# Performance work log

Measured on AMD Instinct MI355X. Metric: run time of the kernel, lower is better.

Reference implementation:

```python
import jax, jax.numpy as jnp
import numpy as np

PATCH = 5
DIM = 256
HEADS = 8
EPS = 1e-5


def split_patches(t, p):
    # t: [B,H,W,C] -> overlapping patches [B,H,W,p,p,C], stride 1, zero-pad p//2
    pad = p // 2
    tp = jnp.pad(t, ((0, 0), (pad, pad), (pad, pad), (0, 0)))
    H, W = t.shape[1], t.shape[2]
    rows = jnp.arange(H)[:, None] + jnp.arange(p)[None, :]  # [H,p]
    cols = jnp.arange(W)[:, None] + jnp.arange(p)[None, :]  # [W,p]
    return tp[:, rows[:, None, :, None], cols[None, :, None, :], :]


def layernorm(v, g, b):
    mu = jnp.mean(v, axis=-1, keepdims=True)
    var = jnp.var(v, axis=-1, keepdims=True)
    return (v - mu) * jax.lax.rsqrt(var + EPS) * g + b


def mha(q, k, v, w, b, mask):
    # w: [4,D,D] stacked (Wq,Wk,Wv,Wo), b: [4,D]; q:[N,Lq,D], k,v:[N,Lk,D]
    N, Lq, D = q.shape
    dh = D // HEADS
    qh = (q @ w[0] + b[0]).reshape(N, Lq, HEADS, dh)
    kh = (k @ w[1] + b[1]).reshape(N, -1, HEADS, dh)
    vh = (v @ w[2] + b[2]).reshape(N, -1, HEADS, dh)
    sc = jnp.einsum('nqhd,nkhd->nhqk', qh, kh) * (1.0 / float(np.sqrt(dh)))
    if mask is not None:
        sc = jnp.where(mask, sc, jnp.asarray(-1e9, sc.dtype))
    a = jax.nn.softmax(sc, axis=-1)
    o = jnp.einsum('nhqk,nkhd->nqhd', a, vh).reshape(N, Lq, D)
    return o @ w[3] + b[3], a


def setup_inputs() -> dict:
    key = jax.random.key(0)
    ks = jax.random.split(key, 10)
    B, H, W, D = 1, 64, 64, DIM
    x = jax.random.normal(ks[0], (B, H, W, D), dtype=jnp.float32)
    memory = jax.random.normal(ks[1], (B, H, W, D), dtype=jnp.float32)
    active_nodes = jax.random.randint(ks[2], (B, H, W), 0, 2).astype(bool)
    s = 0.05
    return {
        'x': x, 'memory': memory, 'active_nodes': active_nodes,
        'attn_w': jax.random.normal(ks[3], (4, D, D), dtype=jnp.float32) * s,
        'attn_b': jnp.zeros((4, D), dtype=jnp.float32),
        'pattn_w': jax.random.normal(ks[4], (4, D, D), dtype=jnp.float32) * s,
        'pattn_b': jnp.zeros((4, D), dtype=jnp.float32),
        'ff_w1': jax.random.normal(ks[5], (D, 2 * D), dtype=jnp.float32) * s,
        'ff_b1': jnp.zeros((2 * D,), dtype=jnp.float32),
        'ff_w2': jax.random.normal(ks[6], (2 * D, D), dtype=jnp.float32) * s,
        'ff_b2': jnp.zeros((D,), dtype=jnp.float32),
        'ln_g': jnp.ones((3, D), dtype=jnp.float32),   # norm1, norm2, norm3
        'ln_b': jnp.zeros((3, D), dtype=jnp.float32),
    }


def reference(x, memory, active_nodes, attn_w, attn_b, pattn_w, pattn_b,
              ff_w1, ff_b1, ff_w2, ff_b2, ln_g, ln_b):
    B, H, W, D = x.shape
    p = PATCH
    center = p // 2
    L = p * p
    cp = L // 2  # flattened center point

    act = active_nodes[..., None]                      # [B,H,W,1] bool
    ap = split_patches(act, p)                         # [B,H,W,p,p,1]
    # faithful to source: zeroes the entire patch at GRID position (center,center)
    ap = ap.at[:, center, center].set(False)
    wo_center = jnp.any(ap.reshape(B, H, W, L, 1), axis=3)  # [B,H,W,1]
    act = jnp.logical_and(wo_center, act)
    ap = split_patches(act, p)                         # recomputed with updated mask

    xp = split_patches(x, p) * ap                      # zero inactive neighbors
    xp = xp.reshape(B, H, W, L, D)
    mp = split_patches(memory, p).reshape(B, H, W, L, D)
    mask = ap[..., 0].reshape(B, H, W, L)

    N = B * H * W
    keys = xp.reshape(N, L, D)
    mem = mp.reshape(N, L, D)
    q = keys[:, cp:cp + 1, :]                          # [N,1,D]
    m = mask.reshape(N, L)[:, None, None, :]           # [N,1,1,L]

    # EncoderLayer (eval mode: dropout = identity)
    s_, attn = mha(q, keys, keys, attn_w, attn_b, m)
    s = layernorm(q + s_, ln_g[0], ln_b[0])            # norm1
    s_, _ = mha(s, mem, mem, pattn_w, pattn_b, None)
    s = layernorm(s + s_, ln_g[2], ln_b[2])            # norm3
    ff = jax.nn.relu(s @ ff_w1 + ff_b1) @ ff_w2 + ff_b2
    s = layernorm(s + ff, ln_g[1], ln_b[1])            # norm2

    out = jnp.where(act, s[:, 0, :].reshape(B, H, W, D), jnp.asarray(0.0, x.dtype))
    return out, act[..., 0]
```

## Files before the change

### kernel.cpp

```cpp
#include <hip/hip_runtime.h>
#include <math.h>

#define D 256
#define H2 512
#define HEADS 8
#define L 25
#define GH 64
#define GW 64
#define NN 4096
#define EPS 1e-5f
#define SCALE 0.17677669529663687f
#define NND 1048576

typedef __attribute__((ext_vector_type(8))) short short8;
typedef __attribute__((ext_vector_type(4))) short short4v;
typedef __attribute__((ext_vector_type(4))) float f32x4;

__device__ __forceinline__ bool act_at(const int* __restrict__ active, int h, int w) {
    if (h < 0 || h >= GH || w < 0 || w >= GW) return false;
    if (h == 2 && w == 2) return false;
    return active[h * GW + w] != 0;
}

__device__ __forceinline__ unsigned short f2b(float f) {
    unsigned u = __float_as_uint(f);
    u += 0x7fffu + ((u >> 16) & 1u);
    return (unsigned short)(u >> 16);
}
__device__ __forceinline__ float b2f(short v) {
    return __uint_as_float(((unsigned)(unsigned short)v) << 16);
}

__device__ __forceinline__ void dma16(const unsigned short* g, unsigned short* l) {
    __builtin_amdgcn_global_load_lds(
        (const __attribute__((address_space(1))) unsigned int*)g,
        (__attribute__((address_space(3))) unsigned int*)l, 16, 0, 0);
}

__global__ __launch_bounds__(256)
void prep_kernel(const float* __restrict__ x, const float* __restrict__ mem,
                 const int* __restrict__ active,
                 const float* __restrict__ attn_w, const float* __restrict__ pattn_w,
                 const float* __restrict__ ff_w1, const float* __restrict__ ff_w2,
                 const float* __restrict__ pattn_b,
                 unsigned short* __restrict__ xmB, unsigned short* __restrict__ memB,
                 unsigned short* __restrict__ wB,
                 unsigned short* __restrict__ k2bias, unsigned short* __restrict__ v2bias) {
    const int tid = threadIdx.x;
    const int bid = blockIdx.x;
    if (bid < 192) {
        __shared__ float tile[64][65];
        const float* src; unsigned short* dst;
        int i0, n0, srcLen, dstLen;
        if (bid < 128) {
            int mat = bid >> 4, t16 = bid & 15;
            i0 = (t16 >> 2) * 64; n0 = (t16 & 3) * 64;
            src = (mat < 4) ? (attn_w + mat * 65536) : (pattn_w + (mat - 4) * 65536);
            dst = wB + mat * 65536;
            srcLen = 256; dstLen = 256;
        } else if (bid < 160) {
            int t = bid - 128;
            i0 = (t >> 3) * 64; n0 = (t & 7) * 64;
            src = ff_w1; dst = wB + 524288;
            srcLen = 512; dstLen = 256;
        } else {
            int t = bid - 160;
            i0 = (t >> 2) * 64; n0 = (t & 3) * 64;
            src = ff_w2; dst = wB + 655360;
            srcLen = 256; dstLen = 512;
        }
        int c = tid & 63, r4 = tid >> 6;
        for (int rr = 0; rr < 64; rr += 4)
            tile[rr + r4][c] = src[(size_t)(i0 + rr + r4) * srcLen + n0 + c];
        __syncthreads();
        for (int rr = 0; rr < 64; rr += 4) {
            int r = rr + r4;
            dst[(size_t)(n0 + r) * dstLen + i0 + c] = f2b(tile[c][r]);
        }
    } else {
        const int t0 = (bid - 192) * 256 + tid;
        for (int t = t0; t < 524800; t += 512 * 256) {
            if (t < 262144) {
                int n = t >> 6;
                bool a = act_at(active, n >> 6, n & 63);
                float4 v = ((const float4*)x)[t];
                ushort4 u;
                u.x = f2b(a ? v.x : 0.0f); u.y = f2b(a ? v.y : 0.0f);
                u.z = f2b(a ? v.z : 0.0f); u.w = f2b(a ? v.w : 0.0f);
                ((ushort4*)xmB)[t] = u;
            } else if (t < 524288) {
                int tt = t - 262144;
                float4 v = ((const float4*)mem)[tt];
                ushort4 u;
                u.x = f2b(v.x); u.y = f2b(v.y); u.z = f2b(v.z); u.w = f2b(v.w);
                ((ushort4*)memB)[tt] = u;
            } else {
                int tt = t - 524288;
                if (tt < 256) k2bias[tt] = f2b(pattn_b[256 + tt]);
                else          v2bias[tt - 256] = f2b(pattn_b[512 + (tt - 256)]);
            }
        }
    }
}

__global__ __launch_bounds__(256)
void proj_gemm(const unsigned short* __restrict__ xmB,
               const unsigned short* __restrict__ memB,
               const unsigned short* __restrict__ wB,
               const float* __restrict__ attn_b, const float* __restrict__ pattn_b,
               unsigned short* __restrict__ q1b, unsigned short* __restrict__ k1b,
               unsigned short* __restrict__ v1b, unsigned short* __restrict__ k2b,
               unsigned short* __restrict__ v2b) {
    const int s  = blockIdx.y >> 2;
    const int n0 = (blockIdx.y & 3) * 64;
    const unsigned short* A  = (s < 3) ? xmB : memB;
    const int wtIdx = (s < 3) ? s : (s + 2);
    const unsigned short* WT = wB + (size_t)wtIdx * 65536;
    const float* bias = (s < 3) ? (attn_b + s * 256) : (pattn_b + (s - 2) * 256);
    unsigned short* outB;
    switch (s) { case 0: outB = q1b; break; case 1: outB = k1b; break;
                 case 2: outB = v1b; break; case 3: outB = k2b; break;
                 default: outB = v2b; }

    const int tid = threadIdx.x;
    const int wave = tid >> 6, lane = tid & 63;
    const int m0 = blockIdx.x * 64 + wave * 16;
    const int lr = lane & 15;
    const int lk = (lane >> 4) << 3;
    f32x4 acc[4] = {};
    const unsigned short* arow = A  + (size_t)(m0 + lr) * 256 + lk;
    const unsigned short* brow = WT + (size_t)(n0 + lr) * 256 + lk;
    #pragma unroll
    for (int kk = 0; kk < 256; kk += 32) {
        short8 a = *(const short8*)(arow + kk);
        #pragma unroll
        for (int nf = 0; nf < 4; ++nf) {
            short8 b = *(const short8*)(brow + (size_t)nf * 16 * 256 + kk);
            acc[nf] = __builtin_amdgcn_mfma_f32_16x16x32_bf16(a, b, acc[nf], 0, 0, 0);
        }
    }
    const int rbase = m0 + ((lane >> 4) << 2);
    #pragma unroll
    for (int nf = 0; nf < 4; ++nf) {
        int c = n0 + nf * 16 + lr;
        float bc = bias[c];
        #pragma unroll
        for (int jj = 0; jj < 4; ++jj)
            outB[(size_t)(rbase + jj) * 256 + c] = f2b(acc[nf][jj] + bc);
    }
}

#define BK_OFF   0
#define BV_OFF   51200
#define WGT_OFF  102400
#define T1B_OFF  115200
#define SB_OFF   123648
#define HB_OFF   132096
#define ACT_OFF  148736
#define REDA_OFF 148864
#define REDB_OFF 149888
#define STAT_OFF 150912
#define SMEM_SZ  151040

__device__ __forceinline__ int union_row(int c, int h, int w0, int fallback) {
    int u = c >> 5;
    int r = u / 20;
    int hh = h - 2 + r, ww = w0 - 2 + (u - r * 20);
    bool ib = ((unsigned)hh < GH) && ((unsigned)ww < GW);
    return ib ? ((hh << 6) | ww) : fallback;
}

__device__ __forceinline__ void dma_union(const unsigned short* __restrict__ base,
                                          int h, int w0, int fallback,
                                          unsigned short* dstLds, int tid) {
    #pragma unroll
    for (int k = 0; k < 4; ++k) {
        int c = tid + k * 1024;
        if (c < 3200) {
            int row = union_row(c, h, w0, fallback);
            dma16(base + (size_t)row * 256 + (c & 31) * 8, dstLds + (size_t)c * 8);
        }
    }
}

__global__ __launch_bounds__(1024)
void fused_kernel(const int* __restrict__ active, const float* __restrict__ x,
                  const unsigned short* __restrict__ wB,
                  const float* __restrict__ attn_b, const float* __restrict__ pattn_b,
                  const float* __restrict__ ff_b1, const float* __restrict__ ff_b2,
                  const float* __restrict__ ln_g, const float* __restrict__ ln_b,
                  const unsigned short* __restrict__ q1b,
                  const unsigned short* __restrict__ k1b,
                  const unsigned short* __restrict__ v1b,
                  const unsigned short* __restrict__ k2b,
                  const unsigned short* __restrict__ v2b,
                  float* __restrict__ out) {
    extern __shared__ __align__(16) char smem[];
    unsigned short (*bufK)[256] = (unsigned short(*)[256])(smem + BK_OFF);
    unsigned short (*bufV)[256] = (unsigned short(*)[256])(smem + BV_OFF);
    float (*wgt)[8][25]         = (float(*)[8][25])(smem + WGT_OFF);
    unsigned short (*T1b)[264]  = (unsigned short(*)[264])(smem + T1B_OFF);
    unsigned short (*Sb)[264]   = (unsigned short(*)[264])(smem + SB_OFF);
    unsigned short (*Hb)[520]   = (unsigned short(*)[520])(smem + HB_OFF);
    unsigned char* actU         = (unsigned char*)(smem + ACT_OFF);
    float (*redA)[16]           = (float(*)[16])(smem + REDA_OFF);
    float (*redB)[16]           = (float(*)[16])(smem + REDB_OFF);
    float (*stats)[2]           = (float(*)[2])(smem + STAT_OFF);

    const int tid = threadIdx.x;
    const int wv = tid >> 6, lane = tid & 63;
    const int lr = lane & 15, qi = lane >> 4;
    const int m = wv;
    const int g8 = lane >> 3;
    const int bid = ((blockIdx.x & 7) << 5) | (blockIdx.x >> 3);
    const int n0 = bid * 16;
    const int h = n0 >> 6, w0 = n0 & 63;

    dma_union(k1b, h, w0, 0, (unsigned short*)(smem + BK_OFF), tid);
    dma_union(v1b, h, w0, 0, (unsigned short*)(smem + BV_OFF), tid);
    if (tid < 100) {
        int r = tid / 20;
        int hh = h - 2 + r, ww = w0 - 2 + (tid - r * 20);
        actU[tid] = act_at(active, hh, ww) ? 1 : 0;
    }
    __syncthreads();

    {
        short4v qv = *(const short4v*)(q1b + (size_t)(n0 + m) * 256 + lane * 4);
        float q[4];
        #pragma unroll
        for (int j = 0; j < 4; ++j) q[j] = b2f(qv[j]);
        #pragma unroll 5
        for (int l = 0; l < L; ++l) {
            int u = (l / 5) * 20 + m + (l % 5);
            short4v kv = *(const short4v*)&bufK[u][lane * 4];
            float p = q[0] * b2f(kv[0]);
            #pragma unroll
            for (int j = 1; j < 4; ++j) p = fmaf(q[j], b2f(kv[j]), p);
            p += __shfl_xor(p, 1); p += __shfl_xor(p, 2); p += __shfl_xor(p, 4);
            float sv = actU[u] ? p * SCALE : -1e30f;
            if ((lane & 7) == 0) wgt[m][g8][l] = sv;
        }
    }
    __syncthreads();

    dma_union(k2b, h, w0, NN, (unsigned short*)(smem + BK_OFF), tid);
    if (tid < 128) {
        int mm = tid >> 3, hd = tid & 7;
        float mx = -1e30f;
        for (int l = 0; l < L; ++l) mx = fmaxf(mx, wgt[mm][hd][l]);
        float sum = 0.0f;
        for (int l = 0; l < L; ++l) { float e = expf(wgt[mm][hd][l] - mx); wgt[mm][hd][l] = e; sum += e; }
        float inv = 1.0f / sum;
        for (int l = 0; l < L; ++l) wgt[mm][hd][l] *= inv;
    }
    __syncthreads();

    {
        float o[4] = {0.f, 0.f, 0.f, 0.f};
        #pragma unroll 5
        for (int l = 0; l < L; ++l) {
            int u = (l / 5) * 20 + m + (l % 5);
            if (actU[u]) {
                float wt = wgt[m][g8][l];
                short4v v4 = *(const short4v*)&bufV[u][lane * 4];
                #pragma unroll
                for (int j = 0; j < 4; ++j) o[j] = fmaf(wt, b2f(v4[j]), o[j]);
            }
        }
        unsigned short u8[4];
        #pragma unroll
        for (int j = 0; j < 4; ++j) u8[j] = f2b(o[j]);
        *(uint2*)&T1b[m][lane * 4] = *(uint2*)u8;
    }
    __syncthreads();

    float sreg[4];
    {
        dma_union(v2b, h, w0, NN, (unsigned short*)(smem + BV_OFF), tid);
        const unsigned short* Wo1T = wB + 3 * 65536;
        f32x4 acc = {};
        #pragma unroll
        for (int kk = 0; kk < 256; kk += 32) {
            short8 a = *(const short8*)&T1b[lr][qi * 8 + kk];
            short8 b = *(const short8*)(Wo1T + (size_t)(wv * 16 + lr) * 256 + qi * 8 + kk);
            acc = __builtin_amdgcn_mfma_f32_16x16x32_bf16(a, b, acc, 0, 0, 0);
        }
        const int c = wv * 16 + lr;
        float bc = attn_b[768 + c];
        float v[4], s1[4], s2[4];
        #pragma unroll
        for (int jj = 0; jj < 4; ++jj) {
            int row = n0 + qi * 4 + jj;
            float vv = acc[jj] + bc + x[(size_t)row * D + c];
            v[jj] = vv; s1[jj] = vv; s2[jj] = vv * vv;
        }
        #pragma unroll
        for (int jj = 0; jj < 4; ++jj) {
            #pragma unroll
            for (int off = 1; off < 16; off <<= 1) {
                s1[jj] += __shfl_xor(s1[jj], off);
                s2[jj] += __shfl_xor(s2[jj], off);
            }
        }
        if (lr == 0) {
            #pragma unroll
            for (int jj = 0; jj < 4; ++jj) { redA[qi*4+jj][wv] = s1[jj]; redB[qi*4+jj][wv] = s2[jj]; }
        }
        __syncthreads();
        if (tid < 16) {
            float a1 = 0.f, a2 = 0.f;
            #pragma unroll
            for (int q8 = 0; q8 < 16; ++q8) { a1 += redA[tid][q8]; a2 += redB[tid][q8]; }
            float mu = a1 * (1.0f / D);
            float var = a2 * (1.0f / D) - mu * mu;
            stats[tid][0] = mu; stats[tid][1] = rsqrtf(var + EPS);
        }
        __syncthreads();
        float gg = ln_g[c], bb = ln_b[c];
        #pragma unroll
        for (int jj = 0; jj < 4; ++jj) {
            int ridx = qi * 4 + jj;
            float ov = (v[jj] - stats[ridx][0]) * stats[ridx][1] * gg + bb;
            sreg[jj] = ov;
            Sb[ridx][c] = f2b(ov);
        }
    }
    __syncthreads();

    float q2[4];
    {
        const unsigned short* Wq2T = wB + 4 * 65536;
        f32x4 acc = {};
        #pragma unroll
        for (int kk = 0; kk < 256; kk += 32) {
            short8 a = *(const short8*)&Sb[lr][qi * 8 + kk];
            short8 b = *(const short8*)(Wq2T + (size_t)(wv * 16 + lr) * 256 + qi * 8 + kk);
            acc = __builtin_amdgcn_mfma_f32_16x16x32_bf16(a, b, acc, 0, 0, 0);
        }
        const int c = wv * 16 + lr;
        float bc = pattn_b[c];
        #pragma unroll
        for (int jj = 0; jj < 4; ++jj)
            T1b[qi * 4 + jj][c] = f2b(acc[jj] + bc);
        __syncthreads();
        short4v qv = *(const short4v*)&T1b[m][lane * 4];
        #pragma unroll
        for (int j = 0; j < 4; ++j) q2[j] = b2f(qv[j]);
    }

    #pragma unroll 5
    for (int l = 0; l < L; ++l) {
        int u = (l / 5) * 20 + m + (l % 5);
        short4v kv = *(const short4v*)&bufK[u][lane * 4];
        float p = q2[0] * b2f(kv[0]);
        #pragma unroll
        for (int j = 1; j < 4; ++j) p = fmaf(q2[j], b2f(kv[j]), p);
        p += __shfl_xor(p, 1); p += __shfl_xor(p, 2); p += __shfl_xor(p, 4);
        if ((lane & 7) == 0) wgt[m][g8][l] = p * SCALE;
    }
    __syncthreads();
    if (tid < 128) {
        int mm = tid >> 3, hd = tid & 7;
        float mx = -1e30f;
        for (int l = 0; l < L; ++l) mx = fmaxf(mx, wgt[mm][hd][l]);
        float sum = 0.0f;
        for (int l = 0; l < L; ++l) { float e = expf(wgt[mm][hd][l] - mx); wgt[mm][hd][l] = e; sum += e; }
        float inv = 1.0f / sum;
        for (int l = 0; l < L; ++l) wgt[mm][hd][l] *= inv;
    }
    __syncthreads();

    {
        float o[4] = {0.f, 0.f, 0.f, 0.f};
        #pragma unroll 5
        for (int l = 0; l < L; ++l) {
            int u = (l / 5) * 20 + m + (l % 5);
            float wt = wgt[m][g8][l];
            short4v v4 = *(const short4v*)&bufV[u][lane * 4];
            #pragma unroll
            for (int j = 0; j < 4; ++j) o[j] = fmaf(wt, b2f(v4[j]), o[j]);
        }
        unsigned short u8[4];
        #pragma unroll
        for (int j = 0; j < 4; ++j) u8[j] = f2b(o[j]);
        *(uint2*)&T1b[m][lane * 4] = *(uint2*)u8;
    }
    __syncthreads();

    float s2reg[4];
    {
        const unsigned short* Wo2T = wB + 7 * 65536;
        f32x4 acc = {};
        #pragma unroll
        for (int kk = 0; kk < 256; kk += 32) {
            short8 a = *(const short8*)&T1b[lr][qi * 8 + kk];
            short8 b = *(const short8*)(Wo2T + (size_t)(wv * 16 + lr) * 256 + qi * 8 + kk);
            acc = __builtin_amdgcn_mfma_f32_16x16x32_bf16(a, b, acc, 0, 0, 0);
        }
        const int c = wv * 16 + lr;
        float bc = pattn_b[768 + c];
        float v[4], s1[4], s2[4];
        #pragma unroll
        for (int jj = 0; jj < 4; ++jj) {
            float vv = acc[jj] + bc + sreg[jj];
            v[jj] = vv; s1[jj] = vv; s2[jj] = vv * vv;
        }
        #pragma unroll
        for (int jj = 0; jj < 4; ++jj) {
            #pragma unroll
            for (int off = 1; off < 16; off <<= 1) {
                s1[jj] += __shfl_xor(s1[jj], off);
                s2[jj] += __shfl_xor(s2[jj], off);
            }
        }
        if (lr == 0) {
            #pragma unroll
            for (int jj = 0; jj < 4; ++jj) { redA[qi*4+jj][wv] = s1[jj]; redB[qi*4+jj][wv] = s2[jj]; }
        }
        __syncthreads();
        if (tid < 16) {
            float a1 = 0.f, a2 = 0.f;
            #pragma unroll
            for (int q8 = 0; q8 < 16; ++q8) { a1 += redA[tid][q8]; a2 += redB[tid][q8]; }
            float mu = a1 * (1.0f / D);
            float var = a2 * (1.0f / D) - mu * mu;
            stats[tid][0] = mu; stats[tid][1] = rsqrtf(var + EPS);
        }
        __syncthreads();
        float gg = ln_g[512 + c], bb = ln_b[512 + c];
        #pragma unroll
        for (int jj = 0; jj < 4; ++jj) {
            int ridx = qi * 4 + jj;
            float ov = (v[jj] - stats[ridx][0]) * stats[ridx][1] * gg + bb;
            s2reg[jj] = ov;
            Sb[ridx][c] = f2b(ov);
        }
    }
    __syncthreads();

    {
        const unsigned short* W1T = wB + 524288;
        f32x4 acc[2] = {};
        #pragma unroll
        for (int kk = 0; kk < 256; kk += 32) {
            short8 a = *(const short8*)&Sb[lr][qi * 8 + kk];
            #pragma unroll
            for (int nf = 0; nf < 2; ++nf) {
                short8 b = *(const short8*)(W1T + (size_t)(wv * 32 + nf * 16 + lr) * 256 + qi * 8 + kk);
                acc[nf] = __builtin_amdgcn_mfma_f32_16x16x32_bf16(a, b, acc[nf], 0, 0, 0);
            }
        }
        #pragma unroll
        for (int nf = 0; nf < 2; ++nf) {
            int c = wv * 32 + nf * 16 + lr;
            float bc = ff_b1[c];
            #pragma unroll
            for (int jj = 0; jj < 4; ++jj)
                Hb[qi * 4 + jj][c] = f2b(fmaxf(acc[nf][jj] + bc, 0.0f));
        }
    }
    __syncthreads();

    {
        const unsigned short* W2T = wB + 655360;
        f32x4 acc = {};
        #pragma unroll
        for (int kk = 0; kk < 512; kk += 32) {
            short8 a = *(const short8*)&Hb[lr][qi * 8 + kk];
            short8 b = *(const short8*)(W2T + (size_t)(wv * 16 + lr) * 512 + qi * 8 + kk);
            acc = __builtin_amdgcn_mfma_f32_16x16x32_bf16(a, b, acc, 0, 0, 0);
        }
        const int c = wv * 16 + lr;
        float bc = ff_b2[c];
        float v[4], s1[4], s2[4];
        #pragma unroll
        for (int jj = 0; jj < 4; ++jj) {
            float vv = acc[jj] + bc + s2reg[jj];
            v[jj] = vv; s1[jj] = vv; s2[jj] = vv * vv;
        }
        #pragma unroll
        for (int jj = 0; jj < 4; ++jj) {
            #pragma unroll
            for (int off = 1; off < 16; off <<= 1) {
                s1[jj] += __shfl_xor(s1[jj], off);
                s2[jj] += __shfl_xor(s2[jj], off);
            }
        }
        if (lr == 0) {
            #pragma unroll
            for (int jj = 0; jj < 4; ++jj) { redA[qi*4+jj][wv] = s1[jj]; redB[qi*4+jj][wv] = s2[jj]; }
        }
        __syncthreads();
        if (tid < 16) {
            float a1 = 0.f, a2 = 0.f;
            #pragma unroll
            for (int q8 = 0; q8 < 16; ++q8) { a1 += redA[tid][q8]; a2 += redB[tid][q8]; }
            float mu = a1 * (1.0f / D);
            float var = a2 * (1.0f / D) - mu * mu;
            stats[tid][0] = mu; stats[tid][1] = rsqrtf(var + EPS);
        }
        __syncthreads();
        bool arow_act[4];
        #pragma unroll
        for (int jj = 0; jj < 4; ++jj) {
            int row = n0 + qi * 4 + jj;
            arow_act[jj] = act_at(active, row >> 6, row & 63);
        }
        float gg = ln_g[256 + c], bb = ln_b[256 + c];
        #pragma unroll
        for (int jj = 0; jj < 4; ++jj) {
            int ridx = qi * 4 + jj;
            float ov = (v[jj] - stats[ridx][0]) * stats[ridx][1] * gg + bb;
            out[(size_t)(n0 + ridx) * D + c] = arow_act[jj] ? ov : 0.0f;
        }
        if (tid < 16) {
            int row = n0 + tid;
            out[(size_t)NND + row] = act_at(active, row >> 6, row & 63) ? 1.0f : 0.0f;
        }
    }
}

extern "C" void kernel_launch(void* const* d_in, const int* in_sizes, int n_in,
                              void* d_out, int out_size, void* d_ws, size_t ws_size,
                              hipStream_t stream) {
    const float* x       = (const float*)d_in[0];
    const float* memory  = (const float*)d_in[1];
    const int*   active  = (const int*)d_in[2];
    const float* attn_w  = (const float*)d_in[3];
    const float* attn_b  = (const float*)d_in[4];
    const float* pattn_w = (const float*)d_in[5];
    const float* pattn_b = (const float*)d_in[6];
    const float* ff_w1   = (const float*)d_in[7];
    const float* ff_b1   = (const float*)d_in[8];
    const float* ff_w2   = (const float*)d_in[9];
    const float* ff_b2   = (const float*)d_in[10];
    const float* ln_g    = (const float*)d_in[11];
    const float* ln_b    = (const float*)d_in[12];
    float* out = (float*)d_out;

    unsigned short* wsb = (unsigned short*)d_ws;
    unsigned short* xmB  = wsb;
    unsigned short* memB = wsb + (size_t)NND;
    unsigned short* wB   = wsb + 2 * (size_t)NND;
    unsigned short* q1b  = wB + 786432;
    unsigned short* k1b  = q1b + (size_t)NND;
    unsigned short* v1b  = k1b + (size_t)NND;
    unsigned short* k2b  = v1b + (size_t)NND;
    unsigned short* v2b  = k2b + (size_t)NND + 256;

    hipFuncSetAttribute(reinterpret_cast<const void*>(fused_kernel),
                        hipFuncAttributeMaxDynamicSharedMemorySize, SMEM_SZ);

    hipLaunchKernelGGL(prep_kernel, dim3(704), dim3(256), 0, stream,
                       x, memory, active, attn_w, pattn_w, ff_w1, ff_w2, pattn_b,
                       xmB, memB, wB, k2b + (size_t)NND, v2b + (size_t)NND);
    hipLaunchKernelGGL(proj_gemm, dim3(64, 20), dim3(256), 0, stream,
                       xmB, memB, wB, attn_b, pattn_b, q1b, k1b, v1b, k2b, v2b);
    hipLaunchKernelGGL(fused_kernel, dim3(256), dim3(1024), SMEM_SZ, stream,
                       active, x, wB, attn_b, pattn_b, ff_b1, ff_b2, ln_g, ln_b,
                       q1b, k1b, v1b, k2b, v2b, out);
}
```

Before: 88.29 us.

## Compute attention softmax in per-lane registers and drop shared score buffer

```diff
diff --git a/kernel.cpp b/kernel.cpp
--- a/kernel.cpp
+++ b/kernel.cpp
@@ -152,15 +152,14 @@
 
 #define BK_OFF   0
 #define BV_OFF   51200
-#define WGT_OFF  102400
-#define T1B_OFF  115200
-#define SB_OFF   123648
-#define HB_OFF   132096
-#define ACT_OFF  148736
-#define REDA_OFF 148864
-#define REDB_OFF 149888
-#define STAT_OFF 150912
-#define SMEM_SZ  151040
+#define T1B_OFF  102400
+#define SB_OFF   110848
+#define HB_OFF   119296
+#define ACT_OFF  135936
+#define REDA_OFF 136064
+#define REDB_OFF 137088
+#define STAT_OFF 138112
+#define SMEM_SZ  138240
 
 __device__ __forceinline__ int union_row(int c, int h, int w0, int fallback) {
     int u = c >> 5;
@@ -198,7 +197,6 @@
     extern __shared__ __align__(16) char smem[];
     unsigned short (*bufK)[256] = (unsigned short(*)[256])(smem + BK_OFF);
     unsigned short (*bufV)[256] = (unsigned short(*)[256])(smem + BV_OFF);
-    float (*wgt)[8][25]         = (float(*)[8][25])(smem + WGT_OFF);
     unsigned short (*T1b)[264]  = (unsigned short(*)[264])(smem + T1B_OFF);
     unsigned short (*Sb)[264]   = (unsigned short(*)[264])(smem + SB_OFF);
     unsigned short (*Hb)[520]   = (unsigned short(*)[520])(smem + HB_OFF);
@@ -211,7 +209,6 @@
     const int wv = tid >> 6, lane = tid & 63;
     const int lr = lane & 15, qi = lane >> 4;
     const int m = wv;
-    const int g8 = lane >> 3;
     const int bid = ((blockIdx.x & 7) << 5) | (blockIdx.x >> 3);
     const int n0 = bid * 16;
     const int h = n0 >> 6, w0 = n0 & 63;
@@ -226,11 +223,14 @@
     __syncthreads();
 
     {
-        short4v qv = *(const short4v*)(q1b + (size_t)(n0 + m) * 256 + lane * 4);
         float q[4];
-        #pragma unroll
-        for (int j = 0; j < 4; ++j) q[j] = b2f(qv[j]);
-        #pragma unroll 5
+        {
+            short4v qv = *(const short4v*)(q1b + (size_t)(n0 + m) * 256 + lane * 4);
+            #pragma unroll
+            for (int j = 0; j < 4; ++j) q[j] = b2f(qv[j]);
+        }
+        float sc[L];
+        #pragma unroll
         for (int l = 0; l < L; ++l) {
             int u = (l / 5) * 20 + m + (l % 5);
             short4v kv = *(const short4v*)&bufK[u][lane * 4];
@@ -238,45 +238,33 @@
             #pragma unroll
             for (int j = 1; j < 4; ++j) p = fmaf(q[j], b2f(kv[j]), p);
             p += __shfl_xor(p, 1); p += __shfl_xor(p, 2); p += __shfl_xor(p, 4);
-            float sv = actU[u] ? p * SCALE : -1e30f;
-            if ((lane & 7) == 0) wgt[m][g8][l] = sv;
-        }
-    }
-    __syncthreads();
-
-    dma_union(k2b, h, w0, NN, (unsigned short*)(smem + BK_OFF), tid);
-    if (tid < 128) {
-        int mm = tid >> 3, hd = tid & 7;
-        float mx = -1e30f;
-        for (int l = 0; l < L; ++l) mx = fmaxf(mx, wgt[mm][hd][l]);
+            sc[l] = actU[u] ? p * SCALE : -1e30f;
+        }
+        float mx = sc[0];
+        #pragma unroll
+        for (int l = 1; l < L; ++l) mx = fmaxf(mx, sc[l]);
         float sum = 0.0f;
-        for (int l = 0; l < L; ++l) { float e = expf(wgt[mm][hd][l] - mx); wgt[mm][hd][l] = e; sum += e; }
+        #pragma unroll
+        for (int l = 0; l < L; ++l) { sc[l] = expf(sc[l] - mx); sum += sc[l]; }
         float inv = 1.0f / sum;
-        for (int l = 0; l < L; ++l) wgt[mm][hd][l] *= inv;
-    }
-    __syncthreads();
-
-    {
         float o[4] = {0.f, 0.f, 0.f, 0.f};
-        #pragma unroll 5
+        #pragma unroll
         for (int l = 0; l < L; ++l) {
             int u = (l / 5) * 20 + m + (l % 5);
-            if (actU[u]) {
-                float wt = wgt[m][g8][l];
-                short4v v4 = *(const short4v*)&bufV[u][lane * 4];
-                #pragma unroll
-                for (int j = 0; j < 4; ++j) o[j] = fmaf(wt, b2f(v4[j]), o[j]);
-            }
+            short4v v4 = *(const short4v*)&bufV[u][lane * 4];
+            #pragma unroll
+            for (int j = 0; j < 4; ++j) o[j] = fmaf(sc[l], b2f(v4[j]), o[j]);
         }
         unsigned short u8[4];
         #pragma unroll
-        for (int j = 0; j < 4; ++j) u8[j] = f2b(o[j]);
+        for (int j = 0; j < 4; ++j) u8[j] = f2b(o[j] * inv);
         *(uint2*)&T1b[m][lane * 4] = *(uint2*)u8;
     }
     __syncthreads();
 
     float sreg[4];
     {
+        dma_union(k2b, h, w0, NN, (unsigned short*)(smem + BK_OFF), tid);
         dma_union(v2b, h, w0, NN, (unsigned short*)(smem + BV_OFF), tid);
         const unsigned short* Wo1T = wB + 3 * 65536;
         f32x4 acc = {};
@@ -349,41 +337,36 @@
         for (int j = 0; j < 4; ++j) q2[j] = b2f(qv[j]);
     }
 
-    #pragma unroll 5
-    for (int l = 0; l < L; ++l) {
-        int u = (l / 5) * 20 + m + (l % 5);
-        short4v kv = *(const short4v*)&bufK[u][lane * 4];
-        float p = q2[0] * b2f(kv[0]);
-        #pragma unroll
-        for (int j = 1; j < 4; ++j) p = fmaf(q2[j], b2f(kv[j]), p);
-        p += __shfl_xor(p, 1); p += __shfl_xor(p, 2); p += __shfl_xor(p, 4);
-        if ((lane & 7) == 0) wgt[m][g8][l] = p * SCALE;
-    }
-    __syncthreads();
-    if (tid < 128) {
-        int mm = tid >> 3, hd = tid & 7;
-        float mx = -1e30f;
-        for (int l = 0; l < L; ++l) mx = fmaxf(mx, wgt[mm][hd][l]);
-        float sum = 0.0f;
-        for (int l = 0; l < L; ++l) { float e = expf(wgt[mm][hd][l] - mx); wgt[mm][hd][l] = e; sum += e; }
-        float inv = 1.0f / sum;
-        for (int l = 0; l < L; ++l) wgt[mm][hd][l] *= inv;
-    }
-    __syncthreads();
-
-    {
-        float o[4] = {0.f, 0.f, 0.f, 0.f};
-        #pragma unroll 5
+    {
+        float sc[L];
+        #pragma unroll
         for (int l = 0; l < L; ++l) {
             int u = (l / 5) * 20 + m + (l % 5);
-            float wt = wgt[m][g8][l];
+            short4v kv = *(const short4v*)&bufK[u][lane * 4];
+            float p = q2[0] * b2f(kv[0]);
+            #pragma unroll
+            for (int j = 1; j < 4; ++j) p = fmaf(q2[j], b2f(kv[j]), p);
+            p += __shfl_xor(p, 1); p += __shfl_xor(p, 2); p += __shfl_xor(p, 4);
+            sc[l] = p * SCALE;
+        }
+        float mx = sc[0];
+        #pragma unroll
+        for (int l = 1; l < L; ++l) mx = fmaxf(mx, sc[l]);
+        float sum = 0.0f;
+        #pragma unroll
+        for (int l = 0; l < L; ++l) { sc[l] = expf(sc[l] - mx); sum += sc[l]; }
+        float inv = 1.0f / sum;
+        float o[4] = {0.f, 0.f, 0.f, 0.f};
+        #pragma unroll
+        for (int l = 0; l < L; ++l) {
+            int u = (l / 5) * 20 + m + (l % 5);
             short4v v4 = *(const short4v*)&bufV[u][lane * 4];
             #pragma unroll
-            for (int j = 0; j < 4; ++j) o[j] = fmaf(wt, b2f(v4[j]), o[j]);
+            for (int j = 0; j < 4; ++j) o[j] = fmaf(sc[l], b2f(v4[j]), o[j]);
         }
         unsigned short u8[4];
         #pragma unroll
-        for (int j = 0; j < 4; ++j) u8[j] = f2b(o[j]);
+        for (int j = 0; j < 4; ++j) u8[j] = f2b(o[j] * inv);
         *(uint2*)&T1b[m][lane * 4] = *(uint2*)u8;
     }
     __syncthreads();
```

New measurement: 86.00 us. 1.03x faster.
